# Performance work log

Measured on AMD Instinct MI355X. Metric: run time of the kernel, lower is better.

Reference implementation:

```python
import jax, jax.numpy as jnp
import numpy as np

B, L, DIM, H = 1, 2048, 1536, 12
HD = DIM // H  # 128
SCALE = HD ** -0.5


def quantize_dequant_int8(t):
    # per-tensor symmetric int8 quantize then float dequantize (same math as torch ref)
    s = jnp.max(jnp.abs(t)) / 127.0
    q = jnp.clip(jnp.round(t / s), -128.0, 127.0)
    return q * s


def setup_inputs() -> dict:
    key = jax.random.key(0)
    ks = jax.random.split(key, 6)
    std = DIM ** -0.5
    return {
        "x": jax.random.normal(ks[0], (B, L, DIM), jnp.float32),
        "Wq": jax.random.normal(ks[1], (DIM, DIM), jnp.float32) * std,
        "Wk": jax.random.normal(ks[2], (DIM, DIM), jnp.float32) * std,
        "Wv": jax.random.normal(ks[3], (DIM, DIM), jnp.float32) * std,
        "Wo": jax.random.normal(ks[4], (DIM, DIM), jnp.float32) * std,
        "bo": jax.random.normal(ks[5], (DIM,), jnp.float32) * 0.01,
    }


def reference(x, Wq, Wk, Wv, Wo, bo):
    b, l, c = x.shape
    # QKV projections (torch Linear: x @ W^T), reshape to [B,H,L,HD]
    q = (x @ Wq.T).reshape(b, l, H, HD).transpose(0, 2, 1, 3)
    k = (x @ Wk.T).reshape(b, l, H, HD).transpose(0, 2, 1, 3)
    v = (x @ Wv.T).reshape(b, l, H, HD).transpose(0, 2, 1, 3)
    # sage-style quantize/dequant around both matmuls
    qd = quantize_dequant_int8(q)
    kd = quantize_dequant_int8(k)
    scores = jnp.einsum('bhqd,bhkd->bhqk', qd, kd) * SCALE
    probs = jax.nn.softmax(scores, axis=-1)
    pd = quantize_dequant_int8(probs)
    vd = quantize_dequant_int8(v)
    out = jnp.einsum('bhqk,bhkd->bhqd', pd, vd)  # [B,H,L,HD]
    out = out.transpose(0, 2, 1, 3).reshape(b, l, c)
    return out @ Wo.T + bo
```

## Files before the change

### kernel.cpp

```cpp
#include <hip/hip_runtime.h>
#include <stdint.h>

#define SEQ 2048
#define DIM 1536
#define NH  12
#define HD  128
#define SCALEF 0.08838834764831845f
#define LDP 40

typedef __attribute__((ext_vector_type(8))) short short8;
typedef __attribute__((ext_vector_type(4))) float floatx4;

#define MFMA16(a, b, c) __builtin_amdgcn_mfma_f32_16x16x32_bf16((a), (b), (c), 0, 0, 0)

__device__ __forceinline__ void async_cp16(const void* g, void* l) {
  __builtin_amdgcn_global_load_lds(
      (__attribute__((address_space(1))) unsigned int*)(g),
      (__attribute__((address_space(3))) unsigned int*)(l), 16, 0, 0);
}

__device__ __forceinline__ unsigned short f2bf(float f) {
  unsigned int u = __float_as_uint(f);
  u = (u + 0x7fff + ((u >> 16) & 1)) >> 16;
  return (unsigned short)u;
}

__device__ __forceinline__ void split8v(const float* x, short8& h, short8& l) {
#pragma unroll
  for (int e = 0; e < 8; e++) {
    unsigned int u = __float_as_uint(x[e]);
    h[e] = (short)(u >> 16);
    float r = x[e] - __uint_as_float(u & 0xFFFF0000u);
    l[e] = (short)f2bf(r);
  }
}
__device__ __forceinline__ void split8(const float* g, short8& h, short8& l) {
  float4 f0 = *(const float4*)g, f1 = *(const float4*)(g + 4);
  float x[8] = {f0.x, f0.y, f0.z, f0.w, f1.x, f1.y, f1.z, f1.w};
  split8v(x, h, l);
}

__global__ __launch_bounds__(256) void k_fill(float* __restrict__ out, int n,
                                              float val) {
  int i = blockIdx.x * 256 + threadIdx.x;
  if (i < n) out[i] = val;
}

__global__ __launch_bounds__(256) void k_gemm_qkv(
    const float* __restrict__ X, const float* __restrict__ Wq,
    const float* __restrict__ Wk, const float* __restrict__ Wv,
    float* __restrict__ qf, float* __restrict__ kf, float* __restrict__ vf,
    unsigned int* __restrict__ scal) {
  __shared__ __align__(16) unsigned short Ah[128 * LDP], Al[128 * LDP];
  __shared__ __align__(16) unsigned short Bh[128 * LDP], Bl[128 * LDP];
  int tid = threadIdx.x, z = blockIdx.z;
  const float* W = (z == 0) ? Wq : (z == 1) ? Wk : Wv;
  float* C = (z == 0) ? qf : (z == 1) ? kf : vf;
  int n0 = blockIdx.x * 128, m0 = blockIdx.y * 128;
  int lane = tid & 63, w = tid >> 6;
  int wr = w >> 1, wc = w & 1, lm = lane & 15, q = lane >> 4;

  floatx4 acc[4][4];
#pragma unroll
  for (int i = 0; i < 4; i++)
#pragma unroll
    for (int j = 0; j < 4; j++) acc[i][j] = (floatx4){0.f, 0.f, 0.f, 0.f};

  int rowA = tid >> 2, c8 = tid & 3;
  for (int k0 = 0; k0 < DIM; k0 += 32) {
    __syncthreads();
#pragma unroll
    for (int i = 0; i < 2; i++) {
      int r = i * 64 + rowA;
      short8 h, l;
      split8(X + (size_t)(m0 + r) * DIM + k0 + c8 * 8, h, l);
      *(short8*)(Ah + r * LDP + c8 * 8) = h;
      *(short8*)(Al + r * LDP + c8 * 8) = l;
      split8(W + (size_t)(n0 + r) * DIM + k0 + c8 * 8, h, l);
      *(short8*)(Bh + r * LDP + c8 * 8) = h;
      *(short8*)(Bl + r * LDP + c8 * 8) = l;
    }
    __syncthreads();
    short8 ah[4], al[4], bh[4], bl[4];
#pragma unroll
    for (int i = 0; i < 4; i++) {
      int r = wr * 64 + i * 16 + lm;
      ah[i] = *(const short8*)(Ah + r * LDP + q * 8);
      al[i] = *(const short8*)(Al + r * LDP + q * 8);
    }
#pragma unroll
    for (int j = 0; j < 4; j++) {
      int r = wc * 64 + j * 16 + lm;
      bh[j] = *(const short8*)(Bh + r * LDP + q * 8);
      bl[j] = *(const short8*)(Bl + r * LDP + q * 8);
    }
#pragma unroll
    for (int i = 0; i < 4; i++)
#pragma unroll
      for (int j = 0; j < 4; j++) {
        acc[i][j] = MFMA16(ah[i], bh[j], acc[i][j]);
        acc[i][j] = MFMA16(ah[i], bl[j], acc[i][j]);
        acc[i][j] = MFMA16(al[i], bh[j], acc[i][j]);
      }
  }
  float am = 0.f;
#pragma unroll
  for (int i = 0; i < 4; i++) {
    int row = m0 + wr * 64 + i * 16 + q * 4;
#pragma unroll
    for (int j = 0; j < 4; j++) {
      int col = n0 + wc * 64 + j * 16 + lm;
#pragma unroll
      for (int r = 0; r < 4; r++) {
        float v = acc[i][j][r];
        C[(size_t)(row + r) * DIM + col] = v;
        am = fmaxf(am, fabsf(v));
      }
    }
  }
#pragma unroll
  for (int mk = 32; mk >= 1; mk >>= 1) am = fmaxf(am, __shfl_xor(am, mk, 64));
  if (lane == 0) atomicMax(&scal[z], __float_as_uint(am));
}

__global__ __launch_bounds__(256) void k_quant_vT(
    const float* __restrict__ vf, const unsigned int* __restrict__ scal,
    unsigned short* __restrict__ nvT) {
  __shared__ float T[64 * 65];
  int h = blockIdx.z, d0 = blockIdx.y * 64, k0 = blockIdx.x * 64;
  float s = __uint_as_float(scal[2]) / 127.f;
  int t = threadIdx.x;
#pragma unroll
  for (int i = 0; i < 16; i++) {
    int idx = i * 256 + t;
    int r = idx >> 6, c = idx & 63;
    float v = vf[(size_t)(k0 + r) * DIM + h * HD + d0 + c];
    T[r * 65 + c] = fminf(fmaxf(rintf(v / s), -128.f), 127.f);
  }
  __syncthreads();
#pragma unroll
  for (int i = 0; i < 16; i++) {
    int idx = i * 256 + t;
    int d = idx >> 6, r = idx & 63;
    nvT[(size_t)(h * HD + d0 + d) * SEQ + k0 + r] = f2bf(T[r * 65 + d]);
  }
}

__global__ __launch_bounds__(256) void k_quant_qk(
    const float* __restrict__ qf, const float* __restrict__ kf,
    const unsigned int* __restrict__ scal,
    unsigned short* __restrict__ nq, unsigned short* __restrict__ nk) {
  int z = blockIdx.y;
  const float* src = z ? kf : qf;
  unsigned short* dst = z ? nk : nq;
  float s = __uint_as_float(scal[z]) / 127.f;
  size_t i = ((size_t)blockIdx.x * 256 + threadIdx.x) * 4;
  float4 v = *(const float4*)(src + i);
  ushort4 o;
  o.x = f2bf(fminf(fmaxf(rintf(v.x / s), -128.f), 127.f));
  o.y = f2bf(fminf(fmaxf(rintf(v.y / s), -128.f), 127.f));
  o.z = f2bf(fminf(fmaxf(rintf(v.z / s), -128.f), 127.f));
  o.w = f2bf(fminf(fmaxf(rintf(v.w / s), -128.f), 127.f));
  *(ushort4*)(dst + i) = o;
}

__global__ __launch_bounds__(256) void k_stats(
    const unsigned short* __restrict__ nq, const unsigned short* __restrict__ nk,
    const unsigned int* __restrict__ scal, float* __restrict__ pstats) {
  __shared__ unsigned short Ks[32 * 128];
  int h = blockIdx.y, tid = threadIdx.x, lane = tid & 63, w = tid >> 6;
  int lm = lane & 15, q = lane >> 4;
  int qb = blockIdx.x & 15, chunk = blockIdx.x >> 4;
  int mb = qb * 128 + w * 32;
  int kbase = chunk * 256;
  float f = (__uint_as_float(scal[0]) / 127.f) *
            (__uint_as_float(scal[1]) / 127.f) * SCALEF;

  short8 aq[2][4];
#pragma unroll
  for (int mi = 0; mi < 2; mi++) {
    const unsigned short* qb_p =
        nq + (size_t)(mb + mi * 16 + lm) * DIM + h * HD + q * 8;
#pragma unroll
    for (int cc = 0; cc < 4; cc++) aq[mi][cc] = *(const short8*)(qb_p + cc * 32);
  }

  float m[2][4], zz[2][4];
// ... 108 lines not shown
        nq + (size_t)(mb + mi * 16 + lm) * DIM + h * HD + q * 8;
#pragma unroll
    for (int cc = 0; cc < 4; cc++) aq[mi][cc] = *(const short8*)(qb_p + cc * 32);
  }
  float M[2][4], invZ[2][4];
#pragma unroll
  for (int mi = 0; mi < 2; mi++)
#pragma unroll
    for (int r = 0; r < 4; r++) {
      int row = mb + mi * 16 + q * 4 + r;
      M[mi][r] = stats[((size_t)h * SEQ + row) * 2];
      invZ[mi][r] = 1.f / stats[((size_t)h * SEQ + row) * 2 + 1];
    }
  floatx4 accO[2][8];
#pragma unroll
  for (int mi = 0; mi < 2; mi++)
#pragma unroll
    for (int j = 0; j < 8; j++) accO[mi][j] = (floatx4){0.f, 0.f, 0.f, 0.f};

  int kbase = chunk * 1024;
  for (int kt = kbase; kt < kbase + 1024; kt += 32) {
    __syncthreads();
#pragma unroll
    for (int i = 0; i < 2; i++) {
      int ch = i * 256 + tid;
      int krow = ch >> 4;
      int gcol = (ch & 15) ^ (krow & 7);
      async_cp16(nk + (size_t)(kt + krow) * DIM + h * HD + gcol * 8,
                 Ks + ch * 8);
      int d = ch >> 2;
      int vcol = (ch & 3) ^ ((d >> 1) & 3);
      async_cp16(nvT + (size_t)(h * HD + d) * SEQ + kt + vcol * 8,
                 Vs + ch * 8);
    }
    __syncthreads();
    short8 bk[2][4];
#pragma unroll
    for (int st = 0; st < 2; st++)
#pragma unroll
      for (int cc = 0; cc < 4; cc++) {
        int phys = (cc * 4 + q) ^ (lm & 7);
        bk[st][cc] = *(const short8*)(Ks + (st * 16 + lm) * 128 + phys * 8);
      }
#pragma unroll
    for (int mi = 0; mi < 2; mi++)
#pragma unroll
      for (int st = 0; st < 2; st++) {
        floatx4 acc = (floatx4){0.f, 0.f, 0.f, 0.f};
#pragma unroll
        for (int cc = 0; cc < 4; cc++) acc = MFMA16(aq[mi][cc], bk[st][cc], acc);
#pragma unroll
        for (int r = 0; r < 4; r++) {
          float t = expf(acc[r] * f - M[mi][r]);
          float n = rintf(t * invZ[mi][r] * inv_sp);
          n = fminf(n, 127.f);
          Pl[w][mi][(q * 4 + r) * 40 + st * 16 + lm] = f2bf(n);
        }
      }
    __syncthreads();
    short8 ap[2];
#pragma unroll
    for (int mi = 0; mi < 2; mi++)
      ap[mi] = *(const short8*)(&Pl[w][mi][lm * 40 + q * 8]);
#pragma unroll
    for (int j = 0; j < 8; j++) {
      int d = j * 16 + lm;
      int vphys = q ^ ((d >> 1) & 3);
      short8 bv = *(const short8*)(Vs + d * 32 + vphys * 8);
#pragma unroll
      for (int mi = 0; mi < 2; mi++) accO[mi][j] = MFMA16(ap[mi], bv, accO[mi][j]);
    }
  }
  float osc = sp * sv;
#pragma unroll
  for (int mi = 0; mi < 2; mi++)
#pragma unroll
    for (int j = 0; j < 8; j++)
#pragma unroll
      for (int r = 0; r < 4; r++)
        attn[(size_t)(mb + mi * 16 + q * 4 + r) * DIM + h * HD + j * 16 + lm] =
            accO[mi][j][r] * osc;
}

__global__ __launch_bounds__(256) void k_gemm_out(
    const float* __restrict__ A0, const float* __restrict__ A1,
    const float* __restrict__ Wo, const float* __restrict__ bo,
    float* __restrict__ out) {
  __shared__ __align__(16) unsigned short Ah[128 * LDP], Al[128 * LDP];
  __shared__ __align__(16) unsigned short Bh[128 * LDP], Bl[128 * LDP];
  int tid = threadIdx.x;
  int n0 = blockIdx.x * 128, m0 = blockIdx.y * 128;
  int lane = tid & 63, w = tid >> 6;
  int wr = w >> 1, wc = w & 1, lm = lane & 15, q = lane >> 4;

  floatx4 acc[4][4];
#pragma unroll
  for (int i = 0; i < 4; i++)
#pragma unroll
    for (int j = 0; j < 4; j++) acc[i][j] = (floatx4){0.f, 0.f, 0.f, 0.f};

  int rowA = tid >> 2, c8 = tid & 3;
  for (int k0 = 0; k0 < DIM; k0 += 32) {
    __syncthreads();
#pragma unroll
    for (int i = 0; i < 2; i++) {
      int r = i * 64 + rowA;
      size_t off = (size_t)(m0 + r) * DIM + k0 + c8 * 8;
      float4 x0 = *(const float4*)(A0 + off), x1 = *(const float4*)(A0 + off + 4);
      float4 y0 = *(const float4*)(A1 + off), y1 = *(const float4*)(A1 + off + 4);
      float xs[8] = {x0.x + y0.x, x0.y + y0.y, x0.z + y0.z, x0.w + y0.w,
                     x1.x + y1.x, x1.y + y1.y, x1.z + y1.z, x1.w + y1.w};
      short8 h, l;
      split8v(xs, h, l);
      *(short8*)(Ah + r * LDP + c8 * 8) = h;
      *(short8*)(Al + r * LDP + c8 * 8) = l;
      split8(Wo + (size_t)(n0 + r) * DIM + k0 + c8 * 8, h, l);
      *(short8*)(Bh + r * LDP + c8 * 8) = h;
      *(short8*)(Bl + r * LDP + c8 * 8) = l;
    }
    __syncthreads();
    short8 ah[4], al[4], bh[4], bl[4];
#pragma unroll
    for (int i = 0; i < 4; i++) {
      int r = wr * 64 + i * 16 + lm;
      ah[i] = *(const short8*)(Ah + r * LDP + q * 8);
      al[i] = *(const short8*)(Al + r * LDP + q * 8);
    }
#pragma unroll
    for (int j = 0; j < 4; j++) {
      int r = wc * 64 + j * 16 + lm;
      bh[j] = *(const short8*)(Bh + r * LDP + q * 8);
      bl[j] = *(const short8*)(Bl + r * LDP + q * 8);
    }
#pragma unroll
    for (int i = 0; i < 4; i++)
#pragma unroll
      for (int j = 0; j < 4; j++) {
        acc[i][j] = MFMA16(ah[i], bh[j], acc[i][j]);
        acc[i][j] = MFMA16(ah[i], bl[j], acc[i][j]);
        acc[i][j] = MFMA16(al[i], bh[j], acc[i][j]);
      }
  }
#pragma unroll
  for (int j = 0; j < 4; j++) {
    int col = n0 + wc * 64 + j * 16 + lm;
    float bias = bo[col];
#pragma unroll
    for (int i = 0; i < 4; i++) {
      int row = m0 + wr * 64 + i * 16 + q * 4;
#pragma unroll
      for (int r = 0; r < 4; r++)
        out[(size_t)(row + r) * DIM + col] = acc[i][j][r] + bias;
    }
  }
}

extern "C" void kernel_launch(void* const* d_in, const int* in_sizes, int n_in,
                              void* d_out, int out_size, void* d_ws, size_t ws_size,
                              hipStream_t stream) {
  float* out = (float*)d_out;
  bool sizes_ok = (n_in >= 6) && in_sizes && in_sizes[0] == SEQ * DIM &&
                  in_sizes[1] == DIM * DIM && in_sizes[2] == DIM * DIM &&
                  in_sizes[3] == DIM * DIM && in_sizes[4] == DIM * DIM &&
                  in_sizes[5] == DIM && out_size == SEQ * DIM;
  if (!sizes_ok) {
    k_fill<<<(out_size + 255) / 256, 256, 0, stream>>>(out, out_size, 1.0f);
    return;
  }
  if (ws_size < 50528272) {
    k_fill<<<(out_size + 255) / 256, 256, 0, stream>>>(out, out_size, 2.0f);
    return;
  }

  const float* x  = (const float*)d_in[0];
  const float* Wq = (const float*)d_in[1];
  const float* Wk = (const float*)d_in[2];
  const float* Wv = (const float*)d_in[3];
  const float* Wo = (const float*)d_in[4];
  const float* bo = (const float*)d_in[5];
  char* ws = (char*)d_ws;

  float* qf = (float*)(ws);
  float* kf = (float*)(ws + 12582912);
  float* vf = (float*)(ws + 25165824);
  unsigned short* nq  = (unsigned short*)(ws + 25165824);
  float* pstats = (float*)(ws + 31457280);
  unsigned short* nvT = (unsigned short*)(ws + 37748736);
  unsigned short* nk  = (unsigned short*)(ws + 44040192);
  float* attn0 = qf;
  float* attn1 = kf;
  float* stats = (float*)(ws + 50331648);
  unsigned int* scal = (unsigned int*)(ws + 50528256);

  hipMemsetAsync(scal, 0, 12, stream);
  hipMemsetAsync(scal + 3, 0x7f, 4, stream);

  k_gemm_qkv<<<dim3(DIM / 128, SEQ / 128, 3), 256, 0, stream>>>(
      x, Wq, Wk, Wv, qf, kf, vf, scal);
  k_quant_vT<<<dim3(SEQ / 64, HD / 64, NH), 256, 0, stream>>>(vf, scal, nvT);
  k_quant_qk<<<dim3((SEQ * DIM) / 1024, 2), 256, 0, stream>>>(qf, kf, scal, nq, nk);
  k_stats<<<dim3(8 * 16, NH), 256, 0, stream>>>(nq, nk, scal, pstats);
  k_merge<<<dim3(NH * SEQ / 256), 256, 0, stream>>>(pstats, stats, scal + 3);
  k_attn<<<dim3(2 * 16, NH), 256, 0, stream>>>(nq, nk, nvT, scal, scal + 3,
                                               stats, attn0, attn1);
  k_gemm_out<<<dim3(DIM / 128, SEQ / 128), 256, 0, stream>>>(attn0, attn1, Wo,
                                                             bo, out);
}
```

Measured before the change: 531.7 us.

## Pre-split activations to bf16 hi/lo tiles and pipeline GEMM loads asynchronously

New kernels split X and the attention output into pre-tiled, swizzled bf16 hi/lo buffers. The QKV and output GEMMs then stream A tiles into LDS with async global-to-LDS copies (triple-buffered) and prefetch W into registers two steps ahead, overlapping loads and splitting with MFMA work. The change also adds block-index remapping for L2 locality and raises wave priority around MFMA. The cost is two extra launches plus a round trip of the split activations through global memory, and the workspace regions it reuses must be free at those points.

```diff
diff --git a/kernel.cpp b/kernel.cpp
--- a/kernel.cpp
+++ b/kernel.cpp
@@ -6,7 +6,6 @@
 #define NH  12
 #define HD  128
 #define SCALEF 0.08838834764831845f
-#define LDP 40
 
 typedef __attribute__((ext_vector_type(8))) short short8;
 typedef __attribute__((ext_vector_type(4))) float floatx4;
@@ -46,17 +45,132 @@
   if (i < n) out[i] = val;
 }
 
+__global__ __launch_bounds__(256) void k_split_x(
+    const float* __restrict__ X, unsigned short* __restrict__ Xh,
+    unsigned short* __restrict__ Xl) {
+  int ks = blockIdx.x, mb = blockIdx.y, tid = threadIdx.x;
+  size_t tb = ((size_t)mb * 48 + ks) * 4096;
+#pragma unroll
+  for (int i = 0; i < 2; i++) {
+    int sidx = i * 256 + tid;
+    int row = sidx >> 2, p = sidx & 3;
+    int c = p ^ ((row >> 1) & 3);
+    short8 h, l;
+    split8(X + (size_t)(mb * 128 + row) * DIM + ks * 32 + c * 8, h, l);
+    *(short8*)(Xh + tb + sidx * 8) = h;
+    *(short8*)(Xl + tb + sidx * 8) = l;
+  }
+}
+
+__global__ __launch_bounds__(256) void k_split_o(
+    const float* __restrict__ A0, const float* __restrict__ A1,
+    unsigned short* __restrict__ Oh, unsigned short* __restrict__ Ol) {
+  int ks = blockIdx.x, mb = blockIdx.y, tid = threadIdx.x;
+  size_t tb = ((size_t)mb * 48 + ks) * 4096;
+#pragma unroll
+  for (int i = 0; i < 2; i++) {
+    int sidx = i * 256 + tid;
+    int row = sidx >> 2, p = sidx & 3;
+    int c = p ^ ((row >> 1) & 3);
+    size_t off = (size_t)(mb * 128 + row) * DIM + ks * 32 + c * 8;
+    float4 x0 = *(const float4*)(A0 + off), x1 = *(const float4*)(A0 + off + 4);
+    float4 y0 = *(const float4*)(A1 + off), y1 = *(const float4*)(A1 + off + 4);
+    float xs[8] = {x0.x + y0.x, x0.y + y0.y, x0.z + y0.z, x0.w + y0.w,
+                   x1.x + y1.x, x1.y + y1.y, x1.z + y1.z, x1.w + y1.w};
+    short8 h, l;
+    split8v(xs, h, l);
+    *(short8*)(Oh + tb + sidx * 8) = h;
+    *(short8*)(Ol + tb + sidx * 8) = l;
+  }
+}
+
+#define COMPUTE_TILE(SA, SB)                                                  \
+  {                                                                           \
+    const unsigned short* Ah_ = Abh + (SA) * 4096;                            \
+    const unsigned short* Al_ = Abl + (SA) * 4096;                            \
+    const unsigned short* Bh_ = Bbh + (SB) * 4096;                            \
+    const unsigned short* Bl_ = Bbl + (SB) * 4096;                            \
+    short8 ah_[4], al_[4], bh_[4], bl_[4];                                    \
+    _Pragma("unroll") for (int i_ = 0; i_ < 4; i_++) {                        \
+      int off_ = (mrbase + i_ * 16) * 32 + phA;                               \
+      ah_[i_] = *(const short8*)(Ah_ + off_);                                 \
+      al_[i_] = *(const short8*)(Al_ + off_);                                 \
+    }                                                                         \
+    _Pragma("unroll") for (int j_ = 0; j_ < 4; j_++) {                        \
+      int off_ = q * 1024 + (wc * 64 + j_ * 16 + lm) * 8;                     \
+      bh_[j_] = *(const short8*)(Bh_ + off_);                                 \
+      bl_[j_] = *(const short8*)(Bl_ + off_);                                 \
+    }                                                                         \
+    __builtin_amdgcn_s_setprio(1);                                            \
+    _Pragma("unroll") for (int i_ = 0; i_ < 4; i_++)                          \
+      _Pragma("unroll") for (int j_ = 0; j_ < 4; j_++) {                      \
+        acc[i_][j_] = MFMA16(ah_[i_], bh_[j_], acc[i_][j_]);                  \
+        acc[i_][j_] = MFMA16(ah_[i_], bl_[j_], acc[i_][j_]);                  \
+        acc[i_][j_] = MFMA16(al_[i_], bh_[j_], acc[i_][j_]);                  \
+      }                                                                       \
+    __builtin_amdgcn_s_setprio(0);                                            \
+  }
+
+#define SPLIT_B(SB, S0x, S1x, S2x, S3x)                                       \
+  {                                                                           \
+    unsigned short* BhN_ = Bbh + (SB) * 4096;                                 \
+    unsigned short* BlN_ = Bbl + (SB) * 4096;                                 \
+    short8 h_, l_;                                                            \
+    {                                                                         \
+      float xs_[8] = {S0x.x, S0x.y, S0x.z, S0x.w,                             \
+                      S1x.x, S1x.y, S1x.z, S1x.w};                            \
+      split8v(xs_, h_, l_);                                                   \
+      *(short8*)(BhN_ + c8 * 1024 + rowA * 8) = h_;                           \
+      *(short8*)(BlN_ + c8 * 1024 + rowA * 8) = l_;                           \
+    }                                                                         \
+    {                                                                         \
+      float xs_[8] = {S2x.x, S2x.y, S2x.z, S2x.w,                             \
+                      S3x.x, S3x.y, S3x.z, S3x.w};                            \
+      split8v(xs_, h_, l_);                                                   \
+      *(short8*)(BhN_ + c8 * 1024 + (64 + rowA) * 8) = h_;                    \
+      *(short8*)(BlN_ + c8 * 1024 + (64 + rowA) * 8) = l_;                    \
+    }                                                                         \
+  }
+
+#define GSTEP(T, SCUR, S0x, S1x, S2x, S3x, L0x, L1x, L2x, L3x)                \
+  {                                                                           \
+    const int t_ = (T), sc_ = (SCUR);                                         \
+    const int sn_ = sc_ >= 1 ? sc_ - 1 : 2;                    \
+    size_t tn_ = tb + (size_t)(t_ + 2) * 4096;                                \
+    async_cp16(XH_ + tn_ + sidx0 * 8, Abh + sn_ * 4096 + sidx0 * 8);          \
+    async_cp16(XL_ + tn_ + sidx0 * 8, Abl + sn_ * 4096 + sidx0 * 8);          \
+    async_cp16(XH_ + tn_ + sidx1 * 8, Abh + sn_ * 4096 + sidx1 * 8);          \
+    async_cp16(XL_ + tn_ + sidx1 * 8, Abl + sn_ * 4096 + sidx1 * 8);          \
+    {                                                                         \
+      int kn_ = (t_ + 2) * 32;                                                \
+      L0x = *(const float4*)(pB0 + kn_);                                      \
+      L1x = *(const float4*)(pB0 + kn_ + 4);                                  \
+      L2x = *(const float4*)(pB1 + kn_);                                      \
+      L3x = *(const float4*)(pB1 + kn_ + 4);                                  \
+    }                                                                         \
+    COMPUTE_TILE(sc_, (t_) & 1);                                              \
+    SPLIT_B((t_ + 1) & 1, S0x, S1x, S2x, S3x);                                \
+    asm volatile("s_waitcnt vmcnt(8) lgkmcnt(0)" ::: "memory");               \
+    __builtin_amdgcn_s_barrier();                                             \
+    __builtin_amdgcn_sched_barrier(0);                                        \
+  }
+
 __global__ __launch_bounds__(256) void k_gemm_qkv(
-    const float* __restrict__ X, const float* __restrict__ Wq,
-    const float* __restrict__ Wk, const float* __restrict__ Wv,
-    float* __restrict__ qf, float* __restrict__ kf, float* __restrict__ vf,
+    const unsigned short* __restrict__ Xh, const unsigned short* __restrict__ Xl,
+    const float* __restrict__ Wq, const float* __restrict__ Wk,
+    const float* __restrict__ Wv, float* __restrict__ qf,
+    float* __restrict__ kf, float* __restrict__ vf,
     unsigned int* __restrict__ scal) {
-  __shared__ __align__(16) unsigned short Ah[128 * LDP], Al[128 * LDP];
-  __shared__ __align__(16) unsigned short Bh[128 * LDP], Bl[128 * LDP];
-  int tid = threadIdx.x, z = blockIdx.z;
+  __shared__ __align__(16) unsigned short Ahs[3][4096], Als[3][4096];
+  __shared__ __align__(16) unsigned short Bhs[2][4096], Bls[2][4096];
+  int tid = threadIdx.x;
+  int L = blockIdx.x + 12 * blockIdx.y + 192 * blockIdx.z;
+  int L2 = (L & 7) * 72 + (L >> 3);
+  int by2 = L2 & 15, rest = L2 >> 4;
+  int bx2 = rest % 12, z = rest / 12;
   const float* W = (z == 0) ? Wq : (z == 1) ? Wk : Wv;
   float* C = (z == 0) ? qf : (z == 1) ? kf : vf;
-  int n0 = blockIdx.x * 128, m0 = blockIdx.y * 128;
+  int n0 = bx2 * 128, m0 = by2 * 128;
   int lane = tid & 63, w = tid >> 6;
   int wr = w >> 1, wc = w & 1, lm = lane & 15, q = lane >> 4;
 
@@ -67,42 +181,55 @@
     for (int j = 0; j < 4; j++) acc[i][j] = (floatx4){0.f, 0.f, 0.f, 0.f};
 
   int rowA = tid >> 2, c8 = tid & 3;
-  for (int k0 = 0; k0 < DIM; k0 += 32) {
-    __syncthreads();
-#pragma unroll
-    for (int i = 0; i < 2; i++) {
-      int r = i * 64 + rowA;
-      short8 h, l;
-      split8(X + (size_t)(m0 + r) * DIM + k0 + c8 * 8, h, l);
-      *(short8*)(Ah + r * LDP + c8 * 8) = h;
-      *(short8*)(Al + r * LDP + c8 * 8) = l;
-      split8(W + (size_t)(n0 + r) * DIM + k0 + c8 * 8, h, l);
-      *(short8*)(Bh + r * LDP + c8 * 8) = h;
-      *(short8*)(Bl + r * LDP + c8 * 8) = l;
-    }
-    __syncthreads();
-    short8 ah[4], al[4], bh[4], bl[4];
-#pragma unroll
-    for (int i = 0; i < 4; i++) {
-      int r = wr * 64 + i * 16 + lm;
-      ah[i] = *(const short8*)(Ah + r * LDP + q * 8);
-      al[i] = *(const short8*)(Al + r * LDP + q * 8);
-    }
-#pragma unroll
-    for (int j = 0; j < 4; j++) {
-      int r = wc * 64 + j * 16 + lm;
-      bh[j] = *(const short8*)(Bh + r * LDP + q * 8);
-      bl[j] = *(const short8*)(Bl + r * LDP + q * 8);
-    }
-#pragma unroll
-    for (int i = 0; i < 4; i++)
-#pragma unroll
-      for (int j = 0; j < 4; j++) {
-        acc[i][j] = MFMA16(ah[i], bh[j], acc[i][j]);
-        acc[i][j] = MFMA16(ah[i], bl[j], acc[i][j]);
-        acc[i][j] = MFMA16(al[i], bh[j], acc[i][j]);
-      }
-  }
+  const float* pB0 = W + (size_t)(n0 + rowA) * DIM + c8 * 8;
+  const float* pB1 = pB0 + (size_t)64 * DIM;
+  size_t tb = (size_t)by2 * 48 * 4096;
+  int sidx0 = tid, sidx1 = 256 + tid;
+  int phA = (q ^ ((lm >> 1) & 3)) * 8;
+  int mrbase = wr * 64 + lm;
+  unsigned short* Abh = &Ahs[0][0];
+  unsigned short* Abl = &Als[0][0];
+  unsigned short* Bbh = &Bhs[0][0];
+  unsigned short* Bbl = &Bls[0][0];
+  const unsigned short* XH_ = Xh;
+  const unsigned short* XL_ = Xl;
+
+  float4 wA0, wA1, wA2, wA3, wB0, wB1, wB2, wB3;
+  wB0 = *(const float4*)(pB0);
+  wB1 = *(const float4*)(pB0 + 4);
+  wB2 = *(const float4*)(pB1);
+  wB3 = *(const float4*)(pB1 + 4);
+  async_cp16(XH_ + tb + sidx0 * 8, Abh + sidx0 * 8);
+  async_cp16(XL_ + tb + sidx0 * 8, Abl + sidx0 * 8);
+  async_cp16(XH_ + tb + sidx1 * 8, Abh + sidx1 * 8);
+  async_cp16(XL_ + tb + sidx1 * 8, Abl + sidx1 * 8);
+  async_cp16(XH_ + tb + 4096 + sidx0 * 8, Abh + 4096 + sidx0 * 8);
+  async_cp16(XL_ + tb + 4096 + sidx0 * 8, Abl + 4096 + sidx0 * 8);
+  async_cp16(XH_ + tb + 4096 + sidx1 * 8, Abh + 4096 + sidx1 * 8);
+  async_cp16(XL_ + tb + 4096 + sidx1 * 8, Abl + 4096 + sidx1 * 8);
+  wA0 = *(const float4*)(pB0 + 32);
+  wA1 = *(const float4*)(pB0 + 36);
+  wA2 = *(const float4*)(pB1 + 32);
+  wA3 = *(const float4*)(pB1 + 36);
+  SPLIT_B(0, wB0, wB1, wB2, wB3);
+  asm volatile("s_waitcnt vmcnt(8) lgkmcnt(0)" ::: "memory");
+  __builtin_amdgcn_s_barrier();
+  __builtin_amdgcn_sched_barrier(0);
+
+  int scur = 0;
+  for (int p = 0; p < 23; ++p) {
+    GSTEP(2 * p, scur, wA0, wA1, wA2, wA3, wB0, wB1, wB2, wB3);
+    scur = (scur + 1 == 3) ? 0 : scur + 1;
+    GSTEP(2 * p + 1, scur, wB0, wB1, wB2, wB3, wA0, wA1, wA2, wA3);
+    scur = (scur + 1 == 3) ? 0 : scur + 1;
+  }
+  COMPUTE_TILE(1, 0);
+  SPLIT_B(1, wA0, wA1, wA2, wA3);
+  asm volatile("s_waitcnt lgkmcnt(0)" ::: "memory");
+  __builtin_amdgcn_s_barrier();
+  __builtin_amdgcn_sched_barrier(0);
+  COMPUTE_TILE(2, 1);
+
   float am = 0.f;
 #pragma unroll
   for (int i = 0; i < 4; i++) {
@@ -378,13 +505,16 @@
 }
 
 __global__ __launch_bounds__(256) void k_gemm_out(
-    const float* __restrict__ A0, const float* __restrict__ A1,
+    const unsigned short* __restrict__ Oh, const unsigned short* __restrict__ Ol,
     const float* __restrict__ Wo, const float* __restrict__ bo,
     float* __restrict__ out) {
-  __shared__ __align__(16) unsigned short Ah[128 * LDP], Al[128 * LDP];
-  __shared__ __align__(16) unsigned short Bh[128 * LDP], Bl[128 * LDP];
+  __shared__ __align__(16) unsigned short Ahs[3][4096], Als[3][4096];
+  __shared__ __align__(16) unsigned short Bhs[2][4096], Bls[2][4096];
   int tid = threadIdx.x;
-  int n0 = blockIdx.x * 128, m0 = blockIdx.y * 128;
+  int L = blockIdx.x + 12 * blockIdx.y;
+  int L2 = (L & 7) * 24 + (L >> 3);
+  int by2 = L2 & 15, bx2 = L2 >> 4;
+  int n0 = bx2 * 128, m0 = by2 * 128;
   int lane = tid & 63, w = tid >> 6;
   int wr = w >> 1, wc = w & 1, lm = lane & 15, q = lane >> 4;
 
@@ -395,47 +525,55 @@
     for (int j = 0; j < 4; j++) acc[i][j] = (floatx4){0.f, 0.f, 0.f, 0.f};
 
   int rowA = tid >> 2, c8 = tid & 3;
-  for (int k0 = 0; k0 < DIM; k0 += 32) {
-    __syncthreads();
-#pragma unroll
-    for (int i = 0; i < 2; i++) {
-      int r = i * 64 + rowA;
-      size_t off = (size_t)(m0 + r) * DIM + k0 + c8 * 8;
-      float4 x0 = *(const float4*)(A0 + off), x1 = *(const float4*)(A0 + off + 4);
-      float4 y0 = *(const float4*)(A1 + off), y1 = *(const float4*)(A1 + off + 4);
-      float xs[8] = {x0.x + y0.x, x0.y + y0.y, x0.z + y0.z, x0.w + y0.w,
-                     x1.x + y1.x, x1.y + y1.y, x1.z + y1.z, x1.w + y1.w};
-      short8 h, l;
-      split8v(xs, h, l);
-      *(short8*)(Ah + r * LDP + c8 * 8) = h;
-      *(short8*)(Al + r * LDP + c8 * 8) = l;
-      split8(Wo + (size_t)(n0 + r) * DIM + k0 + c8 * 8, h, l);
-      *(short8*)(Bh + r * LDP + c8 * 8) = h;
-      *(short8*)(Bl + r * LDP + c8 * 8) = l;
-    }
-    __syncthreads();
-    short8 ah[4], al[4], bh[4], bl[4];
-#pragma unroll
-    for (int i = 0; i < 4; i++) {
-      int r = wr * 64 + i * 16 + lm;
-      ah[i] = *(const short8*)(Ah + r * LDP + q * 8);
-      al[i] = *(const short8*)(Al + r * LDP + q * 8);
-    }
-#pragma unroll
-    for (int j = 0; j < 4; j++) {
-      int r = wc * 64 + j * 16 + lm;
-      bh[j] = *(const short8*)(Bh + r * LDP + q * 8);
-      bl[j] = *(const short8*)(Bl + r * LDP + q * 8);
-    }
-#pragma unroll
-    for (int i = 0; i < 4; i++)
-#pragma unroll
-      for (int j = 0; j < 4; j++) {
-        acc[i][j] = MFMA16(ah[i], bh[j], acc[i][j]);
-        acc[i][j] = MFMA16(ah[i], bl[j], acc[i][j]);
-        acc[i][j] = MFMA16(al[i], bh[j], acc[i][j]);
-      }
-  }
+  const float* pB0 = Wo + (size_t)(n0 + rowA) * DIM + c8 * 8;
+  const float* pB1 = pB0 + (size_t)64 * DIM;
+  size_t tb = (size_t)by2 * 48 * 4096;
+  int sidx0 = tid, sidx1 = 256 + tid;
+  int phA = (q ^ ((lm >> 1) & 3)) * 8;
+  int mrbase = wr * 64 + lm;
+  unsigned short* Abh = &Ahs[0][0];
+  unsigned short* Abl = &Als[0][0];
+  unsigned short* Bbh = &Bhs[0][0];
+  unsigned short* Bbl = &Bls[0][0];
+  const unsigned short* XH_ = Oh;
+  const unsigned short* XL_ = Ol;
+
+  float4 wA0, wA1, wA2, wA3, wB0, wB1, wB2, wB3;
+  wB0 = *(const float4*)(pB0);
+  wB1 = *(const float4*)(pB0 + 4);
+  wB2 = *(const float4*)(pB1);
+  wB3 = *(const float4*)(pB1 + 4);
+  async_cp16(XH_ + tb + sidx0 * 8, Abh + sidx0 * 8);
+  async_cp16(XL_ + tb + sidx0 * 8, Abl + sidx0 * 8);
+  async_cp16(XH_ + tb + sidx1 * 8, Abh + sidx1 * 8);
+  async_cp16(XL_ + tb + sidx1 * 8, Abl + sidx1 * 8);
+  async_cp16(XH_ + tb + 4096 + sidx0 * 8, Abh + 4096 + sidx0 * 8);
+  async_cp16(XL_ + tb + 4096 + sidx0 * 8, Abl + 4096 + sidx0 * 8);
+  async_cp16(XH_ + tb + 4096 + sidx1 * 8, Abh + 4096 + sidx1 * 8);
+  async_cp16(XL_ + tb + 4096 + sidx1 * 8, Abl + 4096 + sidx1 * 8);
+  wA0 = *(const float4*)(pB0 + 32);
+  wA1 = *(const float4*)(pB0 + 36);
+  wA2 = *(const float4*)(pB1 + 32);
+  wA3 = *(const float4*)(pB1 + 36);
+  SPLIT_B(0, wB0, wB1, wB2, wB3);
+  asm volatile("s_waitcnt vmcnt(8) lgkmcnt(0)" ::: "memory");
+  __builtin_amdgcn_s_barrier();
+  __builtin_amdgcn_sched_barrier(0);
+
+  int scur = 0;
+  for (int p = 0; p < 23; ++p) {
+    GSTEP(2 * p, scur, wA0, wA1, wA2, wA3, wB0, wB1, wB2, wB3);
+    scur = (scur + 1 == 3) ? 0 : scur + 1;
+    GSTEP(2 * p + 1, scur, wB0, wB1, wB2, wB3, wA0, wA1, wA2, wA3);
+    scur = (scur + 1 == 3) ? 0 : scur + 1;
+  }
+  COMPUTE_TILE(1, 0);
+  SPLIT_B(1, wA0, wA1, wA2, wA3);
+  asm volatile("s_waitcnt lgkmcnt(0)" ::: "memory");
+  __builtin_amdgcn_s_barrier();
+  __builtin_amdgcn_sched_barrier(0);
+  COMPUTE_TILE(2, 1);
+
 #pragma unroll
   for (int j = 0; j < 4; j++) {
     int col = n0 + wc * 64 + j * 16 + lm;
@@ -482,6 +620,10 @@
   float* pstats = (float*)(ws + 31457280);
   unsigned short* nvT = (unsigned short*)(ws + 37748736);
   unsigned short* nk  = (unsigned short*)(ws + 44040192);
+  unsigned short* Xh = nvT;
+  unsigned short* Xl = nk;
+  unsigned short* Oh = nvT;
+  unsigned short* Ol = nk;
   float* attn0 = qf;
   float* attn1 = kf;
   float* stats = (float*)(ws + 50331648);
@@ -490,14 +632,15 @@
   hipMemsetAsync(scal, 0, 12, stream);
   hipMemsetAsync(scal + 3, 0x7f, 4, stream);
 
+  k_split_x<<<dim3(48, 16), 256, 0, stream>>>(x, Xh, Xl);
   k_gemm_qkv<<<dim3(DIM / 128, SEQ / 128, 3), 256, 0, stream>>>(
-      x, Wq, Wk, Wv, qf, kf, vf, scal);
+      Xh, Xl, Wq, Wk, Wv, qf, kf, vf, scal);
   k_quant_vT<<<dim3(SEQ / 64, HD / 64, NH), 256, 0, stream>>>(vf, scal, nvT);
   k_quant_qk<<<dim3((SEQ * DIM) / 1024, 2), 256, 0, stream>>>(qf, kf, scal, nq, nk);
   k_stats<<<dim3(8 * 16, NH), 256, 0, stream>>>(nq, nk, scal, pstats);
   k_merge<<<dim3(NH * SEQ / 256), 256, 0, stream>>>(pstats, stats, scal + 3);
   k_attn<<<dim3(2 * 16, NH), 256, 0, stream>>>(nq, nk, nvT, scal, scal + 3,
                                                stats, attn0, attn1);
-  k_gemm_out<<<dim3(DIM / 128, SEQ / 128), 256, 0, stream>>>(attn0, attn1, Wo,
-                                                             bo, out);
-}
+  k_split_o<<<dim3(48, 16), 256, 0, stream>>>(attn0, attn1, Oh, Ol);
+  k_gemm_out<<<dim3(DIM / 128, SEQ / 128), 256, 0, stream>>>(Oh, Ol, Wo, bo, out);
+}
```

Measured after the change: 519.3 us. -2.3%, faster.

## Pre-split activations to bf16 tiles and pipeline GEMMs with async LDS loads

Applied to the files above, without the earlier changes.

Adds pre-pass kernels that split X and the summed attention output into swizzled bf16 hi/lo tile buffers. The QKV and output GEMMs now use 512-thread blocks with 256x128 tiles, a triple-buffered async global-to-LDS pipeline for A and double-buffered register-staged B. The MFMA phases are interleaved with barriers, priority hints and a remapped block order for L2 locality. The aim is to stop recomputing the hi/lo split on every tile and to overlap memory traffic with MFMA work. In exchange it adds two extra kernel launches, extra workspace traffic, and hand-tuned waitcnt logic that is fragile.

```diff
diff --git a/kernel.cpp b/kernel.cpp
--- a/kernel.cpp
+++ b/kernel.cpp
@@ -6,7 +6,6 @@
 #define NH  12
 #define HD  128
 #define SCALEF 0.08838834764831845f
-#define LDP 40
 
 typedef __attribute__((ext_vector_type(8))) short short8;
 typedef __attribute__((ext_vector_type(4))) float floatx4;
@@ -46,17 +45,221 @@
   if (i < n) out[i] = val;
 }
 
-__global__ __launch_bounds__(256) void k_gemm_qkv(
-    const float* __restrict__ X, const float* __restrict__ Wq,
-    const float* __restrict__ Wk, const float* __restrict__ Wv,
-    float* __restrict__ qf, float* __restrict__ kf, float* __restrict__ vf,
+__global__ __launch_bounds__(256) void k_split_x(
+    const float* __restrict__ X, unsigned short* __restrict__ Xh,
+    unsigned short* __restrict__ Xl) {
+  int ks = blockIdx.x, mb = blockIdx.y, tid = threadIdx.x;
+  size_t tb = ((size_t)mb * 48 + ks) * 8192;
+#pragma unroll
+  for (int i = 0; i < 4; i++) {
+    int sidx = i * 256 + tid;
+    int row = sidx >> 2, p = sidx & 3;
+    int c = p ^ ((row >> 1) & 3);
+    short8 h, l;
+    split8(X + (size_t)(mb * 256 + row) * DIM + ks * 32 + c * 8, h, l);
+    *(short8*)(Xh + tb + sidx * 8) = h;
+    *(short8*)(Xl + tb + sidx * 8) = l;
+  }
+}
+
+__global__ __launch_bounds__(256) void k_split_o(
+    const float* __restrict__ A0, const float* __restrict__ A1,
+    unsigned short* __restrict__ Oh, unsigned short* __restrict__ Ol) {
+  int ks = blockIdx.x, mb = blockIdx.y, tid = threadIdx.x;
+  size_t tb = ((size_t)mb * 48 + ks) * 8192;
+#pragma unroll
+  for (int i = 0; i < 4; i++) {
+    int sidx = i * 256 + tid;
+    int row = sidx >> 2, p = sidx & 3;
+    int c = p ^ ((row >> 1) & 3);
+    size_t off = (size_t)(mb * 256 + row) * DIM + ks * 32 + c * 8;
+    float4 x0 = *(const float4*)(A0 + off), x1 = *(const float4*)(A0 + off + 4);
+    float4 y0 = *(const float4*)(A1 + off), y1 = *(const float4*)(A1 + off + 4);
+    float xs[8] = {x0.x + y0.x, x0.y + y0.y, x0.z + y0.z, x0.w + y0.w,
+                   x1.x + y1.x, x1.y + y1.y, x1.z + y1.z, x1.w + y1.w};
+    short8 h, l;
+    split8v(xs, h, l);
+    *(short8*)(Oh + tb + sidx * 8) = h;
+    *(short8*)(Ol + tb + sidx * 8) = l;
+  }
+}
+
+#define MFMA3(I, J, AH, AL, BH, BL)                \
+  do {                                             \
+    acc[I][J] = MFMA16(AH, BH, acc[I][J]);         \
+    acc[I][J] = MFMA16(AH, BL, acc[I][J]);         \
+    acc[I][J] = MFMA16(AL, BH, acc[I][J]);         \
+  } while (0)
+
+#define GSTEP(T, ACUR, BCUR, SP0, SP1, LD0, LD1, DO_STAGE, ENDWAIT)           \
+  {                                                                           \
+    const int t_ = (T);                                                       \
+    const unsigned short* Ah_ = &Ah[0][0] + (ACUR) * 8192;                    \
+    const unsigned short* Al_ = &Al[0][0] + (ACUR) * 8192;                    \
+    const unsigned short* Bh_ = &Bh[0][0] + (BCUR) * 5120;                    \
+    const unsigned short* Bl_ = &Bl[0][0] + (BCUR) * 5120;                    \
+    unsigned short* BhN_ = &Bh[0][0] + ((BCUR) ^ 1) * 5120;                   \
+    unsigned short* BlN_ = &Bl[0][0] + ((BCUR) ^ 1) * 5120;                   \
+                  \
+    if (DO_STAGE) {                                                           \
+      int sn_ = (ACUR) >= 1 ? (ACUR) - 1 : 2;                                 \
+      size_t tn_ = tbase + (size_t)(t_ + 2) * 8192;                           \
+      unsigned short* AhN_ = &Ah[0][0] + sn_ * 8192;                          \
+      unsigned short* AlN_ = &Al[0][0] + sn_ * 8192;                          \
+      async_cp16(XH_ + tn_ + tid * 8, AhN_ + tid * 8);                        \
+      async_cp16(XH_ + tn_ + (512 + tid) * 8, AhN_ + (512 + tid) * 8);        \
+      async_cp16(XL_ + tn_ + tid * 8, AlN_ + tid * 8);                        \
+      async_cp16(XL_ + tn_ + (512 + tid) * 8, AlN_ + (512 + tid) * 8);        \
+      int kn_ = (t_ + 2) * 32;                                                \
+      LD0 = *(const float4*)(pB + kn_);                                       \
+      LD1 = *(const float4*)(pB + kn_ + 4);                                   \
+    }                                                                         \
+    short8 a0h, a0l, a1h, a1l, a2h, a2l, a3h, a3l;                            \
+    short8 b0h, b0l, b1h, b1l, b2h, b2l, b3h, b3l;                            \
+    a0h = *(const short8*)(Ah_ + (mrbase + 0) * 32 + phA);                    \
+    a0l = *(const short8*)(Al_ + (mrbase + 0) * 32 + phA);                    \
+    a1h = *(const short8*)(Ah_ + (mrbase + 16) * 32 + phA);                   \
+    a1l = *(const short8*)(Al_ + (mrbase + 16) * 32 + phA);                   \
+    b0h = *(const short8*)(Bh_ + (nrbase + 0) * 40 + q * 8);                  \
+    b0l = *(const short8*)(Bl_ + (nrbase + 0) * 40 + q * 8);                  \
+    b1h = *(const short8*)(Bh_ + (nrbase + 16) * 40 + q * 8);                 \
+    b1l = *(const short8*)(Bl_ + (nrbase + 16) * 40 + q * 8);                 \
+    __builtin_amdgcn_s_barrier();                                             \
+    asm volatile("s_waitcnt lgkmcnt(0)" ::: "memory");                        \
+    __builtin_amdgcn_sched_barrier(0);                                        \
+    __builtin_amdgcn_s_setprio(1);                                            \
+    MFMA3(0, 0, a0h, a0l, b0h, b0l);                                          \
+    MFMA3(0, 1, a0h, a0l, b1h, b1l);                                          \
+    MFMA3(1, 0, a1h, a1l, b0h, b0l);                                          \
+    MFMA3(1, 1, a1h, a1l, b1h, b1l);                                          \
+    __builtin_amdgcn_s_setprio(0);                                            \
+    __builtin_amdgcn_s_barrier();                                             \
+                     \
+    b2h = *(const short8*)(Bh_ + (nrbase + 32) * 40 + q * 8);                 \
+    b2l = *(const short8*)(Bl_ + (nrbase + 32) * 40 + q * 8);                 \
+    b3h = *(const short8*)(Bh_ + (nrbase + 48) * 40 + q * 8);                 \
+    b3l = *(const short8*)(Bl_ + (nrbase + 48) * 40 + q * 8);                 \
+    {                                                                         \
+      float xs_[8] = {SP0.x, SP0.y, SP0.z, SP0.w,                             \
+                      SP1.x, SP1.y, SP1.z, SP1.w};                            \
+      short8 h_, l_;                                                          \
+      split8v(xs_, h_, l_);                                                   \
+      *(short8*)(BhN_ + rowB * 40 + c8 * 8) = h_;                             \
+      *(short8*)(BlN_ + rowB * 40 + c8 * 8) = l_;                             \
+    }                                                                         \
+    __builtin_amdgcn_s_barrier();                                             \
+    asm volatile("s_waitcnt lgkmcnt(2)" ::: "memory");                        \
+    __builtin_amdgcn_sched_barrier(0);                                        \
+    __builtin_amdgcn_s_setprio(1);                                            \
+    MFMA3(0, 2, a0h, a0l, b2h, b2l);                                          \
+    MFMA3(0, 3, a0h, a0l, b3h, b3l);                                          \
+    MFMA3(1, 2, a1h, a1l, b2h, b2l);                                          \
+    MFMA3(1, 3, a1h, a1l, b3h, b3l);                                          \
+    __builtin_amdgcn_s_setprio(0);                                            \
+    __builtin_amdgcn_s_barrier();                                             \
+                                                  \
+    a2h = *(const short8*)(Ah_ + (mrbase + 32) * 32 + phA);                   \
+    a2l = *(const short8*)(Al_ + (mrbase + 32) * 32 + phA);                   \
+    a3h = *(const short8*)(Ah_ + (mrbase + 48) * 32 + phA);                   \
+    a3l = *(const short8*)(Al_ + (mrbase + 48) * 32 + phA);                   \
+    __builtin_amdgcn_s_barrier();                                             \
+    asm volatile("s_waitcnt lgkmcnt(0)" ::: "memory");                        \
+    __builtin_amdgcn_sched_barrier(0);                                        \
+    __builtin_amdgcn_s_setprio(1);                                            \
+    MFMA3(2, 0, a2h, a2l, b0h, b0l);                                          \
+    MFMA3(2, 1, a2h, a2l, b1h, b1l);                                          \
+    MFMA3(3, 0, a3h, a3l, b0h, b0l);                                          \
+    MFMA3(3, 1, a3h, a3l, b1h, b1l);                                          \
+    __builtin_amdgcn_s_setprio(0);                                            \
+    __builtin_amdgcn_s_barrier();                                             \
+                          \
+    __builtin_amdgcn_s_setprio(1);                                            \
+    MFMA3(2, 2, a2h, a2l, b2h, b2l);                                          \
+    MFMA3(2, 3, a2h, a2l, b3h, b3l);                                          \
+    MFMA3(3, 2, a3h, a3l, b2h, b2l);                                          \
+    MFMA3(3, 3, a3h, a3l, b3h, b3l);                                          \
+    __builtin_amdgcn_s_setprio(0);                                            \
+    asm volatile(ENDWAIT ::: "memory");                                       \
+    __builtin_amdgcn_s_barrier();                                             \
+    __builtin_amdgcn_sched_barrier(0);                                        \
+  }
+
+#define GFINAL(ACUR, BCUR)                                                    \
+  {                                                                           \
+    const unsigned short* Ah_ = &Ah[0][0] + (ACUR) * 8192;                    \
+    const unsigned short* Al_ = &Al[0][0] + (ACUR) * 8192;                    \
+    const unsigned short* Bh_ = &Bh[0][0] + (BCUR) * 5120;                    \
+    const unsigned short* Bl_ = &Bl[0][0] + (BCUR) * 5120;                    \
+    short8 ah_[4], al_[4], bh_[4], bl_[4];                                    \
+    _Pragma("unroll") for (int i_ = 0; i_ < 4; i_++) {                        \
+      ah_[i_] = *(const short8*)(Ah_ + (mrbase + i_ * 16) * 32 + phA);        \
+      al_[i_] = *(const short8*)(Al_ + (mrbase + i_ * 16) * 32 + phA);        \
+      bh_[i_] = *(const short8*)(Bh_ + (nrbase + i_ * 16) * 40 + q * 8);      \
+      bl_[i_] = *(const short8*)(Bl_ + (nrbase + i_ * 16) * 40 + q * 8);      \
+    }                                                                         \
+    asm volatile("s_waitcnt lgkmcnt(0)" ::: "memory");                        \
+    _Pragma("unroll") for (int i_ = 0; i_ < 4; i_++)                          \
+      _Pragma("unroll") for (int j_ = 0; j_ < 4; j_++)                        \
+        MFMA3(i_, j_, ah_[i_], al_[i_], bh_[j_], bl_[j_]);                    \
+  }
+
+#define GEMM_PRO()                                                            \
+  {                                                                           \
+    async_cp16(XH_ + tbase + tid * 8, &Ah[0][0] + tid * 8);                   \
+    async_cp16(XH_ + tbase + (512 + tid) * 8, &Ah[0][0] + (512 + tid) * 8);   \
+    async_cp16(XL_ + tbase + tid * 8, &Al[0][0] + tid * 8);                   \
+    async_cp16(XL_ + tbase + (512 + tid) * 8, &Al[0][0] + (512 + tid) * 8);   \
+    async_cp16(XH_ + tbase + 8192 + tid * 8, &Ah[1][0] + tid * 8);            \
+    async_cp16(XH_ + tbase + 8192 + (512 + tid) * 8,                          \
+               &Ah[1][0] + (512 + tid) * 8);                                  \
+    async_cp16(XL_ + tbase + 8192 + tid * 8, &Al[1][0] + tid * 8);            \
+    async_cp16(XL_ + tbase + 8192 + (512 + tid) * 8,                          \
+               &Al[1][0] + (512 + tid) * 8);                                  \
+    wB0 = *(const float4*)(pB);                                               \
+    wB1 = *(const float4*)(pB + 4);                                           \
+    wA0 = *(const float4*)(pB + 32);                                          \
+    wA1 = *(const float4*)(pB + 36);                                          \
+    float xs_[8] = {wB0.x, wB0.y, wB0.z, wB0.w, wB1.x, wB1.y, wB1.z, wB1.w};  \
+    short8 h_, l_;                                                            \
+    split8v(xs_, h_, l_);                                                     \
+    *(short8*)(&Bh[0][0] + rowB * 40 + c8 * 8) = h_;                          \
+    *(short8*)(&Bl[0][0] + rowB * 40 + c8 * 8) = l_;                          \
+    asm volatile("s_waitcnt vmcnt(2) lgkmcnt(0)" ::: "memory");               \
+    __builtin_amdgcn_s_barrier();                                             \
+    __builtin_amdgcn_sched_barrier(0);                                        \
+  }
+
+#define GEMM_LOOP()                                                           \
+  int acur = 0;                                                               \
+  for (int p = 0; p < 23; ++p) {                                              \
+    GSTEP(2 * p, acur, 0, wA0, wA1, wB0, wB1, 1,                              \
+          "s_waitcnt vmcnt(6) lgkmcnt(0)");                                   \
+    acur = (acur + 1 == 3) ? 0 : acur + 1;                                    \
+    GSTEP(2 * p + 1, acur, 1, wB0, wB1, wA0, wA1, 1,                          \
+          "s_waitcnt vmcnt(6) lgkmcnt(0)");                                   \
+    acur = (acur + 1 == 3) ? 0 : acur + 1;                                    \
+  }                                                                           \
+  GSTEP(46, acur, 0, wA0, wA1, wB0, wB1, 0,                                   \
+        "s_waitcnt vmcnt(0) lgkmcnt(0)");                                     \
+  acur = (acur + 1 == 3) ? 0 : acur + 1;                                      \
+  GFINAL(acur, 1);
+
+__global__ __launch_bounds__(512) void k_gemm_qkv(
+    const unsigned short* __restrict__ Xh, const unsigned short* __restrict__ Xl,
+    const float* __restrict__ Wq, const float* __restrict__ Wk,
+    const float* __restrict__ Wv, float* __restrict__ qf,
+    float* __restrict__ kf, float* __restrict__ vf,
     unsigned int* __restrict__ scal) {
-  __shared__ __align__(16) unsigned short Ah[128 * LDP], Al[128 * LDP];
-  __shared__ __align__(16) unsigned short Bh[128 * LDP], Bl[128 * LDP];
-  int tid = threadIdx.x, z = blockIdx.z;
+  __shared__ __align__(16) unsigned short Ah[3][8192], Al[3][8192];
+  __shared__ __align__(16) unsigned short Bh[2][5120], Bl[2][5120];
+  int tid = threadIdx.x;
+  int L = blockIdx.x;
+  int L2 = (L & 7) * 36 + (L >> 3);
+  int by2 = L2 & 7, nIdx = L2 >> 3;
+  int z = nIdx / 12, bx2 = nIdx % 12;
   const float* W = (z == 0) ? Wq : (z == 1) ? Wk : Wv;
   float* C = (z == 0) ? qf : (z == 1) ? kf : vf;
-  int n0 = blockIdx.x * 128, m0 = blockIdx.y * 128;
+  int n0 = bx2 * 128, m0 = by2 * 256;
   int lane = tid & 63, w = tid >> 6;
   int wr = w >> 1, wc = w & 1, lm = lane & 15, q = lane >> 4;
 
@@ -66,43 +269,19 @@
 #pragma unroll
     for (int j = 0; j < 4; j++) acc[i][j] = (floatx4){0.f, 0.f, 0.f, 0.f};
 
-  int rowA = tid >> 2, c8 = tid & 3;
-  for (int k0 = 0; k0 < DIM; k0 += 32) {
-    __syncthreads();
-#pragma unroll
-    for (int i = 0; i < 2; i++) {
-      int r = i * 64 + rowA;
-      short8 h, l;
-      split8(X + (size_t)(m0 + r) * DIM + k0 + c8 * 8, h, l);
-      *(short8*)(Ah + r * LDP + c8 * 8) = h;
-      *(short8*)(Al + r * LDP + c8 * 8) = l;
-      split8(W + (size_t)(n0 + r) * DIM + k0 + c8 * 8, h, l);
-      *(short8*)(Bh + r * LDP + c8 * 8) = h;
-      *(short8*)(Bl + r * LDP + c8 * 8) = l;
-    }
-    __syncthreads();
-    short8 ah[4], al[4], bh[4], bl[4];
-#pragma unroll
-    for (int i = 0; i < 4; i++) {
-      int r = wr * 64 + i * 16 + lm;
-      ah[i] = *(const short8*)(Ah + r * LDP + q * 8);
-      al[i] = *(const short8*)(Al + r * LDP + q * 8);
-    }
-#pragma unroll
-    for (int j = 0; j < 4; j++) {
-      int r = wc * 64 + j * 16 + lm;
-      bh[j] = *(const short8*)(Bh + r * LDP + q * 8);
-      bl[j] = *(const short8*)(Bl + r * LDP + q * 8);
-    }
-#pragma unroll
-    for (int i = 0; i < 4; i++)
-#pragma unroll
-      for (int j = 0; j < 4; j++) {
-        acc[i][j] = MFMA16(ah[i], bh[j], acc[i][j]);
-        acc[i][j] = MFMA16(ah[i], bl[j], acc[i][j]);
-        acc[i][j] = MFMA16(al[i], bh[j], acc[i][j]);
-      }
-  }
+  int rowB = tid >> 2, c8 = tid & 3;
+  const float* pB = W + (size_t)(n0 + rowB) * DIM + c8 * 8;
+  size_t tbase = (size_t)by2 * 48 * 8192;
+  int phA = (q ^ ((lm >> 1) & 3)) * 8;
+  int mrbase = wr * 64 + lm;
+  int nrbase = wc * 64 + lm;
+  const unsigned short* XH_ = Xh;
+  const unsigned short* XL_ = Xl;
+  float4 wA0, wA1, wB0, wB1;
+
+  GEMM_PRO();
+  GEMM_LOOP();
+
   float am = 0.f;
 #pragma unroll
   for (int i = 0; i < 4; i++) {
@@ -377,14 +556,17 @@
             accO[mi][j][r] * osc;
 }
 
-__global__ __launch_bounds__(256) void k_gemm_out(
-    const float* __restrict__ A0, const float* __restrict__ A1,
+__global__ __launch_bounds__(512) void k_gemm_out(
+    const unsigned short* __restrict__ Oh, const unsigned short* __restrict__ Ol,
     const float* __restrict__ Wo, const float* __restrict__ bo,
     float* __restrict__ out) {
-  __shared__ __align__(16) unsigned short Ah[128 * LDP], Al[128 * LDP];
-  __shared__ __align__(16) unsigned short Bh[128 * LDP], Bl[128 * LDP];
+  __shared__ __align__(16) unsigned short Ah[3][8192], Al[3][8192];
+  __shared__ __align__(16) unsigned short Bh[2][5120], Bl[2][5120];
   int tid = threadIdx.x;
-  int n0 = blockIdx.x * 128, m0 = blockIdx.y * 128;
+  int L = blockIdx.x;
+  int L2 = (L & 7) * 12 + (L >> 3);
+  int by2 = L2 & 7, bx2 = L2 >> 3;
+  int n0 = bx2 * 128, m0 = by2 * 256;
   int lane = tid & 63, w = tid >> 6;
   int wr = w >> 1, wc = w & 1, lm = lane & 15, q = lane >> 4;
 
@@ -394,48 +576,19 @@
 #pragma unroll
     for (int j = 0; j < 4; j++) acc[i][j] = (floatx4){0.f, 0.f, 0.f, 0.f};
 
-  int rowA = tid >> 2, c8 = tid & 3;
-  for (int k0 = 0; k0 < DIM; k0 += 32) {
-    __syncthreads();
-#pragma unroll
-    for (int i = 0; i < 2; i++) {
-      int r = i * 64 + rowA;
-      size_t off = (size_t)(m0 + r) * DIM + k0 + c8 * 8;
-      float4 x0 = *(const float4*)(A0 + off), x1 = *(const float4*)(A0 + off + 4);
-      float4 y0 = *(const float4*)(A1 + off), y1 = *(const float4*)(A1 + off + 4);
-      float xs[8] = {x0.x + y0.x, x0.y + y0.y, x0.z + y0.z, x0.w + y0.w,
-                     x1.x + y1.x, x1.y + y1.y, x1.z + y1.z, x1.w + y1.w};
-      short8 h, l;
-      split8v(xs, h, l);
-      *(short8*)(Ah + r * LDP + c8 * 8) = h;
-      *(short8*)(Al + r * LDP + c8 * 8) = l;
-      split8(Wo + (size_t)(n0 + r) * DIM + k0 + c8 * 8, h, l);
-      *(short8*)(Bh + r * LDP + c8 * 8) = h;
-      *(short8*)(Bl + r * LDP + c8 * 8) = l;
-    }
-    __syncthreads();
-    short8 ah[4], al[4], bh[4], bl[4];
-#pragma unroll
-    for (int i = 0; i < 4; i++) {
-      int r = wr * 64 + i * 16 + lm;
-      ah[i] = *(const short8*)(Ah + r * LDP + q * 8);
-      al[i] = *(const short8*)(Al + r * LDP + q * 8);
-    }
-#pragma unroll
-    for (int j = 0; j < 4; j++) {
-      int r = wc * 64 + j * 16 + lm;
-      bh[j] = *(const short8*)(Bh + r * LDP + q * 8);
-      bl[j] = *(const short8*)(Bl + r * LDP + q * 8);
-    }
-#pragma unroll
-    for (int i = 0; i < 4; i++)
-#pragma unroll
-      for (int j = 0; j < 4; j++) {
-        acc[i][j] = MFMA16(ah[i], bh[j], acc[i][j]);
-        acc[i][j] = MFMA16(ah[i], bl[j], acc[i][j]);
-        acc[i][j] = MFMA16(al[i], bh[j], acc[i][j]);
-      }
-  }
+  int rowB = tid >> 2, c8 = tid & 3;
+  const float* pB = Wo + (size_t)(n0 + rowB) * DIM + c8 * 8;
+  size_t tbase = (size_t)by2 * 48 * 8192;
+  int phA = (q ^ ((lm >> 1) & 3)) * 8;
+  int mrbase = wr * 64 + lm;
+  int nrbase = wc * 64 + lm;
+  const unsigned short* XH_ = Oh;
+  const unsigned short* XL_ = Ol;
+  float4 wA0, wA1, wB0, wB1;
+
+  GEMM_PRO();
+  GEMM_LOOP();
+
 #pragma unroll
   for (int j = 0; j < 4; j++) {
     int col = n0 + wc * 64 + j * 16 + lm;
@@ -482,6 +635,10 @@
   float* pstats = (float*)(ws + 31457280);
   unsigned short* nvT = (unsigned short*)(ws + 37748736);
   unsigned short* nk  = (unsigned short*)(ws + 44040192);
+  unsigned short* Xh = nvT;
+  unsigned short* Xl = nk;
+  unsigned short* Oh = nvT;
+  unsigned short* Ol = nk;
   float* attn0 = qf;
   float* attn1 = kf;
   float* stats = (float*)(ws + 50331648);
@@ -490,14 +647,15 @@
   hipMemsetAsync(scal, 0, 12, stream);
   hipMemsetAsync(scal + 3, 0x7f, 4, stream);
 
-  k_gemm_qkv<<<dim3(DIM / 128, SEQ / 128, 3), 256, 0, stream>>>(
-      x, Wq, Wk, Wv, qf, kf, vf, scal);
+  k_split_x<<<dim3(48, 8), 256, 0, stream>>>(x, Xh, Xl);
+  k_gemm_qkv<<<dim3(288), 512, 0, stream>>>(Xh, Xl, Wq, Wk, Wv, qf, kf, vf,
+                                            scal);
   k_quant_vT<<<dim3(SEQ / 64, HD / 64, NH), 256, 0, stream>>>(vf, scal, nvT);
   k_quant_qk<<<dim3((SEQ * DIM) / 1024, 2), 256, 0, stream>>>(qf, kf, scal, nq, nk);
   k_stats<<<dim3(8 * 16, NH), 256, 0, stream>>>(nq, nk, scal, pstats);
   k_merge<<<dim3(NH * SEQ / 256), 256, 0, stream>>>(pstats, stats, scal + 3);
   k_attn<<<dim3(2 * 16, NH), 256, 0, stream>>>(nq, nk, nvT, scal, scal + 3,
                                                stats, attn0, attn1);
-  k_gemm_out<<<dim3(DIM / 128, SEQ / 128), 256, 0, stream>>>(attn0, attn1, Wo,
-                                                             bo, out);
-}
+  k_split_o<<<dim3(48, 8), 256, 0, stream>>>(attn0, attn1, Oh, Ol);
+  k_gemm_out<<<dim3(96), 512, 0, stream>>>(Oh, Ol, Wo, bo, out);
+}
```

Result: slower. 546.8 us (+2.9%).
